# Performance work log

Hardware: AMD Instinct MI355X
Metric: run time of the kernel (lower is better)

## Reference

```python
import jax, jax.numpy as jnp
import numpy as np

N_VERTICES = 1_000_000
N_EDGES = 16_000_000


def setup_inputs() -> dict:
    key = jax.random.key(0)
    k1, k2, k3, k4 = jax.random.split(key, 4)
    # vertex_attr columns: [A_ii, b_i, x_i]; keep A_ii away from 0 for stable division
    A_ii = jax.random.uniform(k1, (N_VERTICES,), jnp.float32, 1.0, 2.0)
    b_i = jax.random.normal(k2, (N_VERTICES,), jnp.float32)
    x_i = jnp.zeros((N_VERTICES,), jnp.float32)
    vertex_attr = jnp.stack([A_ii, b_i, x_i], axis=1)  # [N, 3]
    # edge_attr columns: [A_ij, c_ij] (c_ij is overwritten on first iteration)
    A_ij = jax.random.normal(k3, (N_EDGES,), jnp.float32) * 0.01
    edge_attr = jnp.stack([A_ij, jnp.zeros_like(A_ij)], axis=1)  # [E, 2]
    edgeij_pair = jax.random.randint(k4, (2, N_EDGES), 0, N_VERTICES, jnp.int64)
    g = jnp.array([0.666], jnp.float32)  # Jacobi damping weight w
    return {"n_iters": 10, "vertex_attr": vertex_attr, "edgeij_pair": edgeij_pair,
            "edge_attr": edge_attr, "g": g}


def reference(n_iters, vertex_attr, edgeij_pair, edge_attr, g):
    # MetaLayer convention: row, col = edge_index; vattr_j = x[col]; scatter to row.
    row = edgeij_pair[0]
    col = edgeij_pair[1]
    A_ii = vertex_attr[:, 0]          # [N]
    b_i = vertex_attr[:, 1]           # [N]
    x0 = vertex_attr[:, 2]            # [N]
    A_ij = edge_attr[:, 0]            # [E]
    w = g[0]
    n = A_ii.shape[0]

    def step(x, _):
        # EdgeUpdate: c_ij = A_ij * x_j ; aggregation: cbar_i = sum_j c_ij
        c_ij = A_ij * x[col]                                     # [E]
        cbar = jax.ops.segment_sum(c_ij, row, num_segments=n)    # [N]
        # VertexUpdate: x <- x + w * (b - cbar) / A_ii
        x_new = x + w * (b_i - cbar) / A_ii
        return x_new, None

    x, _ = jax.lax.scan(step, x0, None, length=n_iters)
    return x.reshape(-1, 1)
```

## Files before the change

kernel.cpp:

```cpp
#include <hip/hip_runtime.h>
#include <hip/hip_fp16.h>

static constexpr int BLK  = 256;
static constexpr int B1   = 256;
static constexpr int BLKW = 1024;
static constexpr int RSH  = 14;
static constexpr int RPB  = 16384;
static constexpr int RMSK = 16383;
static constexpr int NCS  = 4;
static constexpr int CSH  = 18;
static constexpr int NSMAX = 256;

typedef unsigned long long ull;

__global__ void detect_kernel(const ull* __restrict__ rc, int* __restrict__ flag) {
    if (blockIdx.x == 0 && threadIdx.x == 0) {
        int is64 = 1;
        for (int i = 0; i < 8; ++i)
            if (rc[i] >= (1ull << 20)) is64 = 0;
        *flag = is64;
    }
}

__global__ void hist1_kernel(const void* __restrict__ rcv,
                             const int* __restrict__ flag,
                             unsigned int* __restrict__ hist, int ne, int nseg) {
    __shared__ unsigned int lh[NSMAX];
    const int b = blockIdx.x;
    const int chunk = (ne + B1 - 1) / B1;
    const int s = b * chunk, e = min(ne, s + chunk);
    for (int i = threadIdx.x; i < NSMAX; i += BLKW) lh[i] = 0u;
    __syncthreads();
    const int is64 = *flag;
    const ull*          r64 = (const ull*)rcv;
    const unsigned int* r32 = (const unsigned int*)rcv;
    for (int i = s + threadIdx.x; i < e; i += BLKW) {
        unsigned int row, col;
        if (is64) { row = (unsigned int)r64[i]; col = (unsigned int)r64[(size_t)ne + i]; }
        else      { row = r32[i];               col = r32[(size_t)ne + i]; }
        unsigned int seg = (row >> RSH) * NCS + (col >> CSH);
        atomicAdd(&lh[seg], 1u);
    }
    __syncthreads();
    for (int i = threadIdx.x; i < nseg; i += BLKW)
        hist[(size_t)i * B1 + b] = lh[i];
}

__global__ void scan1_kernel(unsigned int* __restrict__ data,
                             unsigned int* __restrict__ part, int n) {
    __shared__ unsigned int s[BLK];
    int t = threadIdx.x;
    int i = blockIdx.x * BLK + t;
    unsigned int v = (i < n) ? data[i] : 0u;
    s[t] = v;
    __syncthreads();
    for (int off = 1; off < BLK; off <<= 1) {
        unsigned int u = (t >= off) ? s[t - off] : 0u;
        __syncthreads();
        s[t] += u;
        __syncthreads();
    }
    if (i < n) data[i] = s[t] - v;
    if (t == BLK - 1) part[blockIdx.x] = s[t];
}

__global__ void scan2_kernel(unsigned int* __restrict__ part, int np) {
    __shared__ unsigned int s[BLK];
    __shared__ unsigned int carry_s;
    int t = threadIdx.x;
    if (t == 0) carry_s = 0u;
    __syncthreads();
    for (int base = 0; base < np; base += BLK) {
        int i = base + t;
        unsigned int v = (i < np) ? part[i] : 0u;
        s[t] = v;
        __syncthreads();
        for (int off = 1; off < BLK; off <<= 1) {
            unsigned int u = (t >= off) ? s[t - off] : 0u;
            __syncthreads();
            s[t] += u;
            __syncthreads();
        }
        unsigned int carry = carry_s;
        if (i < np) part[i] = s[t] - v + carry;
        __syncthreads();
        if (t == BLK - 1) carry_s = carry + s[t];
        __syncthreads();
    }
}

__global__ void scan3_kernel(unsigned int* __restrict__ data,
                             const unsigned int* __restrict__ part, int n) {
    int i = blockIdx.x * BLK + threadIdx.x;
    if (i < n) data[i] += part[blockIdx.x];
}

__global__ void scatter1_kernel(const void* __restrict__ rcv,
                                const float2* __restrict__ eattr,
                                const int* __restrict__ flag,
                                const unsigned int* __restrict__ base,
                                ull* __restrict__ edges, int ne, int nseg) {
    __shared__ unsigned int cur[NSMAX];
    const int b = blockIdx.x;
    const int chunk = (ne + B1 - 1) / B1;
    const int s = b * chunk, e = min(ne, s + chunk);
    for (int i = threadIdx.x; i < nseg; i += BLKW)
        cur[i] = base[(size_t)i * B1 + b];
    __syncthreads();
    const int is64 = *flag;
    const ull*          r64 = (const ull*)rcv;
    const unsigned int* r32 = (const unsigned int*)rcv;
    for (int i = s + threadIdx.x; i < e; i += BLKW) {
        ull row, col;
        if (is64) { row = r64[i]; col = r64[(size_t)ne + i]; }
        else      { row = r32[i]; col = r32[(size_t)ne + i]; }
        float a = eattr[i].x;
        unsigned short h = __half_as_ushort(__float2half(a));
        ull q = (row << 44) | (col << 24) | (ull)h;
        unsigned int seg = (unsigned int)(row >> RSH) * NCS
                         + (unsigned int)(col >> CSH);
        unsigned int pos = atomicAdd(&cur[seg], 1u);
        edges[pos] = q;
    }
}

__global__ void vprep_kernel(const float* __restrict__ vattr,
                             const float* __restrict__ g,
                             float2* __restrict__ vp,
                             float* __restrict__ x0, int nv) {
    int i = blockIdx.x * BLK + threadIdx.x;
    if (i >= nv) return;
    float A = vattr[3 * i + 0];
    float b = vattr[3 * i + 1];
    float x = vattr[3 * i + 2];
    float w = g[0];
    vp[i] = make_float2(w * b / A, w / A);
    x0[i] = x;
}

__global__ __launch_bounds__(BLKW)
void iter_kernel(const unsigned int* __restrict__ base,
                 const ull* __restrict__ edges,
                 const float* __restrict__ xin,
                 float* __restrict__ p,
                 int ne, int nseg, int nprows) {
    __shared__ float acc[RPB];
    const int i = blockIdx.x;
    const int b = i >> 2, cs = i & 3;
    const int t = threadIdx.x;
    #pragma unroll
    for (int k = t; k < RPB; k += BLKW) acc[k] = 0.0f;
    __syncthreads();
    const unsigned int s = base[(size_t)i * B1];
    const unsigned int e = (i == nseg - 1) ? (unsigned int)ne
                                           : base[(size_t)(i + 1) * B1];
    #pragma unroll 4
    for (unsigned int j = s + t; j < e; j += BLKW) {
        ull q = edges[j];
        float a = __half2float(__ushort_as_half((unsigned short)(q & 0xFFFFu)));
        unsigned int col = (unsigned int)(q >> 24) & 0xFFFFFu;
        unsigned int r   = (unsigned int)(q >> 44) & RMSK;
        atomicAdd(&acc[r], a * xin[col]);
    }
    __syncthreads();
    float* plane = p + (size_t)cs * nprows + ((size_t)b << RSH);
    #pragma unroll
    for (int k = t; k < RPB; k += BLKW) plane[k] = acc[k];
}

__global__ void merge_kernel(const float* __restrict__ p,
                             const float2* __restrict__ vp,
                             const float* __restrict__ xin,
                             float* __restrict__ xout, int nv, int nprows) {
    int i = blockIdx.x * BLK + threadIdx.x;
    if (i >= nv) return;
    float c = p[i] + p[(size_t)nprows + i]
            + p[2 * (size_t)nprows + i] + p[3 * (size_t)nprows + i];
    float2 q = vp[i];
    xout[i] = xin[i] + q.x - q.y * c;
}

extern "C" void kernel_launch(void* const* d_in, const int* in_sizes, int n_in,
                              void* d_out, int out_size, void* d_ws, size_t ws_size,
                              hipStream_t stream) {
    const float* vattr = (const float*)d_in[1];
    const void*  eij   = (const void*)d_in[2];
    const float* eattr = (const float*)d_in[3];
    const float* g     = (const float*)d_in[4];
    const int nv = in_sizes[1] / 3;
    const int ne = in_sizes[3] / 2;
    const int n_iters = 10;
    const int nb   = (nv + RMSK) >> RSH;
    const int nseg = nb * NCS;
    const int nh   = nseg * B1;
    const int nprows = nb << RSH;

    char* ws = (char*)d_ws;
    size_t off = 0;
    auto alloc = [&](size_t bytes) -> void* {
        void* p = ws + off;
        off = (off + bytes + 255) & ~(size_t)255;
        return p;
    };
    ull* edges = (ull*)alloc((size_t)ne * 8);
    unsigned int* hist = (unsigned int*)alloc((size_t)nh * 4);
    unsigned int* part = (unsigned int*)alloc(((size_t)(nh + BLK - 1) / BLK) * 4);
    float* p = (float*)alloc((size_t)NCS * nprows * 4);
    float2* vp = (float2*)alloc((size_t)nv * 8);
    float*  xa = (float*) alloc((size_t)nv * 4);
    float*  xb = (float*) alloc((size_t)nv * 4);
    int*  flag = (int*)   alloc(256);

    const int vblocks = (nv + BLK - 1) / BLK;
    const int sblocks = (nh + BLK - 1) / BLK;

    detect_kernel<<<1, 64, 0, stream>>>((const ull*)eij, flag);
    hist1_kernel<<<B1, BLKW, 0, stream>>>(eij, flag, hist, ne, nseg);
    scan1_kernel<<<sblocks, BLK, 0, stream>>>(hist, part, nh);
    scan2_kernel<<<1, BLK, 0, stream>>>(part, sblocks);
    scan3_kernel<<<sblocks, BLK, 0, stream>>>(hist, part, nh);
    scatter1_kernel<<<B1, BLKW, 0, stream>>>(eij, (const float2*)eattr, flag,
                                             hist, edges, ne, nseg);
    vprep_kernel<<<vblocks, BLK, 0, stream>>>(vattr, g, vp, xa, nv);

    float* xin  = xa;
    float* xout = xb;
    for (int it = 0; it < n_iters; ++it) {
        iter_kernel<<<nseg, BLKW, 0, stream>>>(hist, edges, xin, p, ne, nseg,
                                               nprows);
        float* dst = (it == n_iters - 1) ? (float*)d_out : xout;
        merge_kernel<<<vblocks, BLK, 0, stream>>>(p, vp, xin, dst, nv, nprows);
        float* t = xin; xin = dst; xout = t;
    }
}
```

Before: 1.248 ms.

## Fine-bin edges by column chunk and compact to 6-byte edge records

Edges are now binned into 128 column chunks per row block instead of 4, and a new finesort pass sorts each chunk by column sub-bucket in shared memory. Each edge is repacked into a 32-bit row/col word plus a separate fp16 coefficient. The iteration kernel uses 8 column slices, so it reads 6 bytes per edge instead of 8 and gathers x with better locality. The cost is an extra preprocessing kernel, an 8192-entry shared histogram in the hist/scatter kernels, and the merge summing 8 partial planes instead of 4.

```diff
diff --git a/kernel.cpp b/kernel.cpp
--- a/kernel.cpp
+++ b/kernel.cpp
@@ -1,17 +1,20 @@
 #include <hip/hip_runtime.h>
 #include <hip/hip_fp16.h>
 
-static constexpr int BLK  = 256;
-static constexpr int B1   = 256;
-static constexpr int BLKW = 1024;
-static constexpr int RSH  = 14;
-static constexpr int RPB  = 16384;
-static constexpr int RMSK = 16383;
-static constexpr int NCS  = 4;
-static constexpr int CSH  = 18;
-static constexpr int NSMAX = 256;
+static constexpr int BLK   = 256;
+static constexpr int B1    = 256;
+static constexpr int BLKW  = 1024;
+static constexpr int RSH   = 14;
+static constexpr int RPB   = 16384;
+static constexpr int RMSK  = 16383;
+static constexpr int NCH   = 128;
+static constexpr int CHSH  = 13;
+static constexpr int NCS   = 8;
+static constexpr int NSMAX = 8192;
+static constexpr int FCAP  = 3072;
 
 typedef unsigned long long ull;
+typedef unsigned int uint;
 
 __global__ void detect_kernel(const ull* __restrict__ rc, int* __restrict__ flag) {
     if (blockIdx.x == 0 && threadIdx.x == 0) {
@@ -24,38 +27,37 @@
 
 __global__ void hist1_kernel(const void* __restrict__ rcv,
                              const int* __restrict__ flag,
-                             unsigned int* __restrict__ hist, int ne, int nseg) {
-    __shared__ unsigned int lh[NSMAX];
+                             uint* __restrict__ hist, int ne, int nseg) {
+    __shared__ uint lh[NSMAX];
     const int b = blockIdx.x;
     const int chunk = (ne + B1 - 1) / B1;
     const int s = b * chunk, e = min(ne, s + chunk);
     for (int i = threadIdx.x; i < NSMAX; i += BLKW) lh[i] = 0u;
     __syncthreads();
     const int is64 = *flag;
-    const ull*          r64 = (const ull*)rcv;
-    const unsigned int* r32 = (const unsigned int*)rcv;
+    const ull*  r64 = (const ull*)rcv;
+    const uint* r32 = (const uint*)rcv;
     for (int i = s + threadIdx.x; i < e; i += BLKW) {
-        unsigned int row, col;
-        if (is64) { row = (unsigned int)r64[i]; col = (unsigned int)r64[(size_t)ne + i]; }
-        else      { row = r32[i];               col = r32[(size_t)ne + i]; }
-        unsigned int seg = (row >> RSH) * NCS + (col >> CSH);
-        atomicAdd(&lh[seg], 1u);
+        uint row, col;
+        if (is64) { row = (uint)r64[i]; col = (uint)r64[(size_t)ne + i]; }
+        else      { row = r32[i];       col = r32[(size_t)ne + i]; }
+        atomicAdd(&lh[(row >> RSH) * NCH + (col >> CHSH)], 1u);
     }
     __syncthreads();
     for (int i = threadIdx.x; i < nseg; i += BLKW)
         hist[(size_t)i * B1 + b] = lh[i];
 }
 
-__global__ void scan1_kernel(unsigned int* __restrict__ data,
-                             unsigned int* __restrict__ part, int n) {
-    __shared__ unsigned int s[BLK];
+__global__ void scan1_kernel(uint* __restrict__ data,
+                             uint* __restrict__ part, int n) {
+    __shared__ uint s[BLK];
     int t = threadIdx.x;
     int i = blockIdx.x * BLK + t;
-    unsigned int v = (i < n) ? data[i] : 0u;
+    uint v = (i < n) ? data[i] : 0u;
     s[t] = v;
     __syncthreads();
     for (int off = 1; off < BLK; off <<= 1) {
-        unsigned int u = (t >= off) ? s[t - off] : 0u;
+        uint u = (t >= off) ? s[t - off] : 0u;
         __syncthreads();
         s[t] += u;
         __syncthreads();
@@ -64,24 +66,24 @@
     if (t == BLK - 1) part[blockIdx.x] = s[t];
 }
 
-__global__ void scan2_kernel(unsigned int* __restrict__ part, int np) {
-    __shared__ unsigned int s[BLK];
-    __shared__ unsigned int carry_s;
+__global__ void scan2_kernel(uint* __restrict__ part, int np) {
+    __shared__ uint s[BLK];
+    __shared__ uint carry_s;
     int t = threadIdx.x;
     if (t == 0) carry_s = 0u;
     __syncthreads();
     for (int base = 0; base < np; base += BLK) {
         int i = base + t;
-        unsigned int v = (i < np) ? part[i] : 0u;
+        uint v = (i < np) ? part[i] : 0u;
         s[t] = v;
         __syncthreads();
         for (int off = 1; off < BLK; off <<= 1) {
-            unsigned int u = (t >= off) ? s[t - off] : 0u;
+            uint u = (t >= off) ? s[t - off] : 0u;
             __syncthreads();
             s[t] += u;
             __syncthreads();
         }
-        unsigned int carry = carry_s;
+        uint carry = carry_s;
         if (i < np) part[i] = s[t] - v + carry;
         __syncthreads();
         if (t == BLK - 1) carry_s = carry + s[t];
@@ -89,8 +91,8 @@
     }
 }
 
-__global__ void scan3_kernel(unsigned int* __restrict__ data,
-                             const unsigned int* __restrict__ part, int n) {
+__global__ void scan3_kernel(uint* __restrict__ data,
+                             const uint* __restrict__ part, int n) {
     int i = blockIdx.x * BLK + threadIdx.x;
     if (i < n) data[i] += part[blockIdx.x];
 }
@@ -98,9 +100,9 @@
 __global__ void scatter1_kernel(const void* __restrict__ rcv,
                                 const float2* __restrict__ eattr,
                                 const int* __restrict__ flag,
-                                const unsigned int* __restrict__ base,
+                                const uint* __restrict__ base,
                                 ull* __restrict__ edges, int ne, int nseg) {
-    __shared__ unsigned int cur[NSMAX];
+    __shared__ uint cur[NSMAX];
     const int b = blockIdx.x;
     const int chunk = (ne + B1 - 1) / B1;
     const int s = b * chunk, e = min(ne, s + chunk);
@@ -108,8 +110,8 @@
         cur[i] = base[(size_t)i * B1 + b];
     __syncthreads();
     const int is64 = *flag;
-    const ull*          r64 = (const ull*)rcv;
-    const unsigned int* r32 = (const unsigned int*)rcv;
+    const ull*  r64 = (const ull*)rcv;
+    const uint* r32 = (const uint*)rcv;
     for (int i = s + threadIdx.x; i < e; i += BLKW) {
         ull row, col;
         if (is64) { row = r64[i]; col = r64[(size_t)ne + i]; }
@@ -117,10 +119,70 @@
         float a = eattr[i].x;
         unsigned short h = __half_as_ushort(__float2half(a));
         ull q = (row << 44) | (col << 24) | (ull)h;
-        unsigned int seg = (unsigned int)(row >> RSH) * NCS
-                         + (unsigned int)(col >> CSH);
-        unsigned int pos = atomicAdd(&cur[seg], 1u);
+        uint seg = (uint)(row >> RSH) * NCH + (uint)(col >> CHSH);
+        uint pos = atomicAdd(&cur[seg], 1u);
         edges[pos] = q;
+    }
+}
+
+__global__ void finesort_kernel(const ull* __restrict__ edges,
+                                const uint* __restrict__ base,
+                                uint* __restrict__ rc32,
+                                unsigned short* __restrict__ af16,
+                                int ne, int nseg) {
+    __shared__ uint cnt[512];
+    __shared__ uint cur[512];
+    __shared__ uint ss[BLK];
+    __shared__ uint  stage_rc[FCAP];
+    __shared__ unsigned short stage_a[FCAP];
+    const int seg = blockIdx.x;
+    const int t = threadIdx.x;
+    const uint s = base[(size_t)seg * B1];
+    const uint e = (seg == nseg - 1) ? (uint)ne : base[(size_t)(seg + 1) * B1];
+    const uint n = e - s;
+    cnt[2 * t] = 0u; cnt[2 * t + 1] = 0u;
+    __syncthreads();
+    if (n <= (uint)FCAP) {
+        for (uint j = s + t; j < e; j += BLK) {
+            uint col = (uint)(edges[j] >> 24) & 0xFFFFFu;
+            atomicAdd(&cnt[(col >> 4) & 511u], 1u);
+        }
+        __syncthreads();
+        uint v0 = cnt[2 * t], v1 = cnt[2 * t + 1];
+        uint tsum = v0 + v1;
+        ss[t] = tsum;
+        __syncthreads();
+        for (int off = 1; off < BLK; off <<= 1) {
+            uint u = (t >= off) ? ss[t - off] : 0u;
+            __syncthreads();
+            ss[t] += u;
+            __syncthreads();
+        }
+        uint exc = ss[t] - tsum;
+        cur[2 * t] = exc;
+        cur[2 * t + 1] = exc + v0;
+        __syncthreads();
+        for (uint j = s + t; j < e; j += BLK) {
+            ull q = edges[j];
+            uint col = (uint)(q >> 24) & 0xFFFFFu;
+            uint r   = (uint)(q >> 44) & RMSK;
+            uint pos = atomicAdd(&cur[(col >> 4) & 511u], 1u);
+            stage_rc[pos] = (r << 17) | (col & 0x1FFFFu);
+            stage_a[pos]  = (unsigned short)(q & 0xFFFFu);
+        }
+        __syncthreads();
+        for (uint k = t; k < n; k += BLK) {
+            rc32[s + k] = stage_rc[k];
+            af16[s + k] = stage_a[k];
+        }
+    } else {
+        for (uint j = s + t; j < e; j += BLK) {
+            ull q = edges[j];
+            uint col = (uint)(q >> 24) & 0xFFFFFu;
+            uint r   = (uint)(q >> 44) & RMSK;
+            rc32[j] = (r << 17) | (col & 0x1FFFFu);
+            af16[j] = (unsigned short)(q & 0xFFFFu);
+        }
     }
 }
 
@@ -139,31 +201,32 @@
 }
 
 __global__ __launch_bounds__(BLKW)
-void iter_kernel(const unsigned int* __restrict__ base,
-                 const ull* __restrict__ edges,
+void iter_kernel(const uint* __restrict__ segstart,
+                 const uint* __restrict__ rc32,
+                 const unsigned short* __restrict__ af16,
                  const float* __restrict__ xin,
                  float* __restrict__ p,
                  int ne, int nseg, int nprows) {
     __shared__ float acc[RPB];
     const int i = blockIdx.x;
-    const int b = i >> 2, cs = i & 3;
+    const int rb = i >> 3, cs = i & 7;
     const int t = threadIdx.x;
     #pragma unroll
     for (int k = t; k < RPB; k += BLKW) acc[k] = 0.0f;
     __syncthreads();
-    const unsigned int s = base[(size_t)i * B1];
-    const unsigned int e = (i == nseg - 1) ? (unsigned int)ne
-                                           : base[(size_t)(i + 1) * B1];
+    const int seg0 = rb * NCH + cs * (NCH / NCS);
+    const int seg1 = seg0 + (NCH / NCS);
+    const uint s = segstart[(size_t)seg0 * B1];
+    const uint e = (seg1 >= nseg) ? (uint)ne : segstart[(size_t)seg1 * B1];
+    const uint cbase = (uint)cs << 17;
     #pragma unroll 4
-    for (unsigned int j = s + t; j < e; j += BLKW) {
-        ull q = edges[j];
-        float a = __half2float(__ushort_as_half((unsigned short)(q & 0xFFFFu)));
-        unsigned int col = (unsigned int)(q >> 24) & 0xFFFFFu;
-        unsigned int r   = (unsigned int)(q >> 44) & RMSK;
-        atomicAdd(&acc[r], a * xin[col]);
-    }
-    __syncthreads();
-    float* plane = p + (size_t)cs * nprows + ((size_t)b << RSH);
+    for (uint j = s + t; j < e; j += BLKW) {
+        uint rc = rc32[j];
+        float a = __half2float(__ushort_as_half(af16[j]));
+        atomicAdd(&acc[rc >> 17], a * xin[cbase | (rc & 0x1FFFFu)]);
+    }
+    __syncthreads();
+    float* plane = p + (size_t)cs * nprows + ((size_t)rb << RSH);
     #pragma unroll
     for (int k = t; k < RPB; k += BLKW) plane[k] = acc[k];
 }
@@ -174,8 +237,9 @@
                              float* __restrict__ xout, int nv, int nprows) {
     int i = blockIdx.x * BLK + threadIdx.x;
     if (i >= nv) return;
-    float c = p[i] + p[(size_t)nprows + i]
-            + p[2 * (size_t)nprows + i] + p[3 * (size_t)nprows + i];
+    float c = 0.0f;
+    #pragma unroll
+    for (int cs = 0; cs < NCS; ++cs) c += p[(size_t)cs * nprows + i];
     float2 q = vp[i];
     xout[i] = xin[i] + q.x - q.y * c;
 }
@@ -190,10 +254,10 @@
     const int nv = in_sizes[1] / 3;
     const int ne = in_sizes[3] / 2;
     const int n_iters = 10;
-    const int nb   = (nv + RMSK) >> RSH;
-    const int nseg = nb * NCS;
+    const int nrb  = (nv + RMSK) >> RSH;
+    const int nseg = nrb * NCH;
     const int nh   = nseg * B1;
-    const int nprows = nb << RSH;
+    const int nprows = nrb << RSH;
 
     char* ws = (char*)d_ws;
     size_t off = 0;
@@ -203,8 +267,10 @@
         return p;
     };
     ull* edges = (ull*)alloc((size_t)ne * 8);
-    unsigned int* hist = (unsigned int*)alloc((size_t)nh * 4);
-    unsigned int* part = (unsigned int*)alloc(((size_t)(nh + BLK - 1) / BLK) * 4);
+    uint* rc32 = (uint*)alloc((size_t)ne * 4);
+    unsigned short* af16 = (unsigned short*)alloc((size_t)ne * 2);
+    uint* hist = (uint*)alloc((size_t)nh * 4);
+    uint* part = (uint*)alloc(((size_t)(nh + BLK - 1) / BLK) * 4);
     float* p = (float*)alloc((size_t)NCS * nprows * 4);
     float2* vp = (float2*)alloc((size_t)nv * 8);
     float*  xa = (float*) alloc((size_t)nv * 4);
@@ -221,13 +287,14 @@
     scan3_kernel<<<sblocks, BLK, 0, stream>>>(hist, part, nh);
     scatter1_kernel<<<B1, BLKW, 0, stream>>>(eij, (const float2*)eattr, flag,
                                              hist, edges, ne, nseg);
+    finesort_kernel<<<nseg, BLK, 0, stream>>>(edges, hist, rc32, af16, ne, nseg);
     vprep_kernel<<<vblocks, BLK, 0, stream>>>(vattr, g, vp, xa, nv);
 
     float* xin  = xa;
     float* xout = xb;
     for (int it = 0; it < n_iters; ++it) {
-        iter_kernel<<<nseg, BLKW, 0, stream>>>(hist, edges, xin, p, ne, nseg,
-                                               nprows);
+        iter_kernel<<<nrb * NCS, BLKW, 0, stream>>>(hist, rc32, af16, xin, p,
+                                                    ne, nseg, nprows);
         float* dst = (it == n_iters - 1) ? (float*)d_out : xout;
         merge_kernel<<<vblocks, BLK, 0, stream>>>(p, vp, xin, dst, nv, nprows);
         float* t = xin; xin = dst; xout = t;
```

New measurement: 1.598 ms. 1.28x slower.
